# Kernel optimization log

Measured on AMD Instinct MI355X. Metric: run time of the kernel, lower is better.

## Reference

```python
import jax, jax.numpy as jnp
import numpy as np

H, HKV, DH = 16, 8, 128
G = H // HKV
EPS = 1e-6
ROPE_THETA = 1000000.0


def _rms_norm(x, w):
    # RMSNorm over last dim (head_dim)
    var = jnp.mean(x * x, axis=-1, keepdims=True)
    return x * jax.lax.rsqrt(var + EPS) * w


def _rotate_half(x):
    x1, x2 = jnp.split(x, 2, axis=-1)
    return jnp.concatenate([-x2, x1], axis=-1)


def setup_inputs() -> dict:
    key = jax.random.key(0)
    ks = jax.random.split(key, 5)
    B, T, D = 2, 2048, 2048
    s = 0.02
    return {
        "x": jax.random.normal(ks[0], (B, T, D), jnp.float32),
        "wq": jax.random.normal(ks[1], (H * DH, D), jnp.float32) * s,
        "wk": jax.random.normal(ks[2], (HKV * DH, D), jnp.float32) * s,
        "wv": jax.random.normal(ks[3], (HKV * DH, D), jnp.float32) * s,
        "wo": jax.random.normal(ks[4], (D, H * DH), jnp.float32) * s,
        "q_norm_w": jnp.ones((DH,), jnp.float32),
        "k_norm_w": jnp.ones((DH,), jnp.float32),
    }


def reference(x, wq, wk, wv, wo, q_norm_w, k_norm_w):
    B, T, D = x.shape
    # projections (nn.Linear: y = x @ W^T)
    q = (x @ wq.T).reshape(B, T, H, DH).transpose(0, 2, 1, 3)      # [B,H,T,Dh]
    k = (x @ wk.T).reshape(B, T, HKV, DH).transpose(0, 2, 1, 3)    # [B,Hkv,T,Dh]
    v = (x @ wv.T).reshape(B, T, HKV, DH).transpose(0, 2, 1, 3)    # [B,Hkv,T,Dh]

    # QK RMSNorm
    q = _rms_norm(q, q_norm_w)
    k = _rms_norm(k, k_norm_w)

    # RoPE (half-split style), positions 0..T-1
    inv_freq = 1.0 / (ROPE_THETA ** (jnp.arange(0, DH, 2, dtype=jnp.float32) / DH))
    freqs = jnp.arange(T, dtype=jnp.float32)[:, None] * inv_freq[None, :]   # [T,Dh/2]
    emb = jnp.concatenate([freqs, freqs], axis=-1)                           # [T,Dh]
    cos = jnp.cos(emb)[None, None, :, :]
    sin = jnp.sin(emb)[None, None, :, :]
    q = q * cos + _rotate_half(q) * sin
    k = k * cos + _rotate_half(k) * sin

    # GQA attention with fp32 scores and causal mask
    qg = q.reshape(B, HKV, G, T, DH)
    scores = jnp.einsum("bhgtd,bhkd->bhgtk", qg.astype(jnp.float32),
                        k.astype(jnp.float32)) / jnp.sqrt(jnp.float32(DH))
    causal = jnp.tril(jnp.ones((T, T), dtype=bool))[None, None, None, :, :]
    scores = jnp.where(causal, scores, jnp.finfo(jnp.float32).min)
    attn = jax.nn.softmax(scores, axis=-1).astype(x.dtype)
    ctx = jnp.einsum("bhgtk,bhkd->bhgtd", attn, v)                            # [B,Hkv,G,T,Dh]
    out = ctx.reshape(B, H, T, DH).transpose(0, 2, 1, 3).reshape(B, T, H * DH)
    return out @ wo.T
```

## Files before the change

### kernel.cpp

```cpp
#include <hip/hip_runtime.h>
#include <cstdint>

#define Hq 16
#define HKVn 8
#define DHn 128
#define Tn 2048
#define Bn 2
#define Dm 2048
#define BT (Bn*Tn)

typedef __attribute__((ext_vector_type(8))) short bfrag8;
typedef __attribute__((ext_vector_type(4))) float facc4;
typedef __attribute__((ext_vector_type(4))) _Float16 f16x4;
typedef __attribute__((ext_vector_type(8))) _Float16 f16x8;

__device__ __forceinline__ unsigned short f2bf(float f) {
    union { float f; unsigned int u; } v; v.f = f;
    unsigned int u = v.u;
    unsigned int r = (u + 0x7FFFu + ((u >> 16) & 1u)) >> 16;
    return (unsigned short)r;
}

__global__ __launch_bounds__(256) void cvt_kernel(const float* __restrict__ in,
                                                  unsigned short* __restrict__ out, int n4) {
    int i = blockIdx.x * 256 + threadIdx.x;
    if (i < n4) {
        float4 x = ((const float4*)in)[i];
        ushort4 y;
        y.x = f2bf(x.x); y.y = f2bf(x.y); y.z = f2bf(x.z); y.w = f2bf(x.w);
        ((ushort4*)out)[i] = y;
    }
}

__global__ __launch_bounds__(256) void gemm_bt(const unsigned short* __restrict__ A,
                                               const unsigned short* __restrict__ Bm,
                                               float* __restrict__ C,
                                               int M, int N, int K) {
    __shared__ char smem[16384];
    int tid = threadIdx.x;
    int w = tid >> 6, lane = tid & 63, quad = lane >> 4, l15 = lane & 15;
    int wr = w >> 1, wc = w & 1;
    int rowBase = blockIdx.y * 128, colBase = blockIdx.x * 128;
    facc4 acc[4][4];
#pragma unroll
    for (int i = 0; i < 4; i++)
#pragma unroll
        for (int j = 0; j < 4; j++) acc[i][j] = facc4{0.f, 0.f, 0.f, 0.f};

    for (int k0 = 0; k0 < K; k0 += 32) {
        __syncthreads();
#pragma unroll
        for (int issue = 0; issue < 2; issue++) {
            int idx = issue * 256 + tid;
            const unsigned short* ga = A + (size_t)(rowBase + (idx >> 2)) * K + k0 + (idx & 3) * 8;
            __builtin_amdgcn_global_load_lds((const __attribute__((address_space(1))) void*)ga,
                (__attribute__((address_space(3))) void*)(smem + issue * 4096 + w * 1024), 16, 0, 0);
            const unsigned short* gb = Bm + (size_t)(colBase + (idx >> 2)) * K + k0 + (idx & 3) * 8;
            __builtin_amdgcn_global_load_lds((const __attribute__((address_space(1))) void*)gb,
                (__attribute__((address_space(3))) void*)(smem + 8192 + issue * 4096 + w * 1024), 16, 0, 0);
        }
        __syncthreads();
        bfrag8 af[4], bf[4];
#pragma unroll
        for (int i = 0; i < 4; i++)
            af[i] = *(const bfrag8*)(smem + ((wr * 64 + i * 16 + l15) * 32 + quad * 8) * 2);
#pragma unroll
        for (int j = 0; j < 4; j++)
            bf[j] = *(const bfrag8*)(smem + 8192 + ((wc * 64 + j * 16 + l15) * 32 + quad * 8) * 2);
#pragma unroll
        for (int i = 0; i < 4; i++)
#pragma unroll
            for (int j = 0; j < 4; j++)
                acc[i][j] = __builtin_amdgcn_mfma_f32_16x16x32_bf16(af[i], bf[j], acc[i][j], 0, 0, 0);
    }
#pragma unroll
    for (int i = 0; i < 4; i++)
#pragma unroll
        for (int j = 0; j < 4; j++)
#pragma unroll
            for (int r = 0; r < 4; r++) {
                int row = rowBase + wr * 64 + i * 16 + quad * 4 + r;
                int col = colBase + wc * 64 + j * 16 + l15;
                C[(size_t)row * N + col] = acc[i][j][r];
            }
}

__device__ __forceinline__ size_t koff_tiled(int t, int d) {
    int kc = (t >> 4) & 3, l15 = t & 15;
    int f = d >> 5, qd = (d >> 3) & 3, j = d & 7;
    return (size_t)(t >> 6) * 8192 + ((((kc * 4 + f) * 64 + qd * 16 + l15) << 3) + j);
}

__global__ __launch_bounds__(256) void normrope_kernel(const float* __restrict__ qkv,
                                                       const float* __restrict__ qw,
                                                       const float* __restrict__ kw,
                                                       unsigned short* __restrict__ q_bf,
                                                       unsigned short* __restrict__ k_bf) {
    int gw = (blockIdx.x * 256 + threadIdx.x) >> 6;
    int lane = threadIdx.x & 63;
    const float* src; const float* wn; float scale; int t;
    bool isq = (gw < BT * Hq);
    unsigned short* qdst = nullptr; unsigned short* kbase = nullptr;
    if (isq) {
        int bt = gw >> 4, h = gw & 15;
        int b = bt >> 11; t = bt & 2047;
        src = qkv + (size_t)bt * 4096 + h * 128;
        qdst = q_bf + ((size_t)(b * Hq + h) * Tn + t) * 128;
        wn = qw; scale = 0.08838834764831845f;
    } else {
        int g2 = gw - BT * Hq;
        int bt = g2 >> 3, hk = g2 & 7;
        int b = bt >> 11; t = bt & 2047;
        src = qkv + (size_t)bt * 4096 + 2048 + hk * 128;
        kbase = k_bf + (size_t)(b * HKVn + hk) * Tn * 128;
        wn = kw; scale = 1.0f;
    }
    float x0 = src[lane], x1 = src[lane + 64];
    float ss = x0 * x0 + x1 * x1;
#pragma unroll
    for (int off = 32; off > 0; off >>= 1) ss += __shfl_xor(ss, off);
    float inv = rsqrtf(ss * (1.0f / 128.0f) + 1e-6f);
    float n0 = x0 * inv * wn[lane];
    float n1 = x1 * inv * wn[lane + 64];
    float fr = exp2f(-(float)lane * 0.3114307588956902f);
    float ang = (float)t * fr;
    float c = cosf(ang), s = sinf(ang);
    float y0 = (n0 * c - n1 * s) * scale;
    float y1 = (n1 * c + n0 * s) * scale;
    if (isq) {
        qdst[lane] = f2bf(y0);
        qdst[lane + 64] = f2bf(y1);
    } else {
        kbase[koff_tiled(t, lane)] = f2bf(y0);
        kbase[koff_tiled(t, lane + 64)] = f2bf(y1);
    }
}

__global__ __launch_bounds__(256) void vtrans_kernel(const float* __restrict__ qkv,
                                                     _Float16* __restrict__ vT) {
    __shared__ _Float16 tile[64 * 128];
    int tid = threadIdx.x;
    int t64 = blockIdx.x & 31, hk = (blockIdx.x >> 5) & 7, b = blockIdx.x >> 8;
    int t0 = t64 * 64;
#pragma unroll
    for (int i = 0; i < 8; i++) {
        int ix = i * 256 + tid;
        int tl = ix >> 5, dc = (ix & 31) * 4;
        float4 v = *(const float4*)(qkv + (size_t)(b * Tn + t0 + tl) * 4096 + 3072 + hk * 128 + dc);
        tile[tl * 128 + dc + 0] = (_Float16)v.x;
        tile[tl * 128 + dc + 1] = (_Float16)v.y;
        tile[tl * 128 + dc + 2] = (_Float16)v.z;
        tile[tl * 128 + dc + 3] = (_Float16)v.w;
    }
    __syncthreads();
    _Float16* out = vT + (((size_t)(b * HKVn + hk) * 32 + t64) * 8192);
#pragma unroll
    for (int i = 0; i < 4; i++) {
        int oc = i * 256 + tid;
        int dblk = oc >> 7, kcp = (oc >> 6) & 1, qd = (oc >> 4) & 3, l15 = oc & 15;
        f16x8 st;
#pragma unroll
        for (int e = 0; e < 8; e++) {
            int hh = e >> 2, jj = e & 3;
            int t = kcp * 32 + hh * 16 + qd * 4 + jj;
            int d = dblk * 16 + l15;
            st[e] = tile[t * 128 + d];
        }
        *(f16x8*)(out + oc * 8) = st;
    }
}

__global__ __launch_bounds__(256, 2) void attn_kernel(const unsigned short* __restrict__ q_bf,
                                                      const unsigned short* __restrict__ k_glob,
                                                      const _Float16* __restrict__ v_glob,
                                                      unsigned short* __restrict__ ctx) {
    __shared__ char smem[65536];
    int tid = threadIdx.x;
    int w = tid >> 6, lane = tid & 63, quad = lane >> 4, l15 = lane & 15;
    int bid = blockIdx.x;
    int u = bid & 255, halfg = bid >> 8;
    int j = u & 7, h = (u >> 3) & 15, b = (u >> 7) & 1;
    int qblk = halfg ? j : 15 - j;
    int hkv = h >> 1;
    int qb = qblk * 128;
    int qw0 = qb + w * 32;

    const unsigned short* qp = q_bf + (size_t)(b * Hq + h) * Tn * 128;
    const unsigned short* ktile = k_glob + (size_t)(b * HKVn + hkv) * 32 * 8192;
    const _Float16* vtile = v_glob + (size_t)(b * HKVn + hkv) * 32 * 8192;

    bfrag8 qf[2][4];
#pragma unroll
    for (int g = 0; g < 2; g++) {
        int row = qw0 + g * 16 + l15;
#pragma unroll
        for (int f = 0; f < 4; f++)
            qf[g][f] = *(const bfrag8*)(qp + (size_t)row * 128 + f * 32 + quad * 8);
    }

    facc4 o0[8], o1[8];
#pragma unroll
    for (int jj = 0; jj < 8; jj++) { o0[jj] = facc4{0.f,0.f,0.f,0.f}; o1[jj] = facc4{0.f,0.f,0.f,0.f}; }
    float m0 = -__builtin_inff(), m1 = -__builtin_inff(), l0 = 0.f, l1 = 0.f;

    int nkb = qb / 64 + 2;

    {
#pragma unroll
        for (int i = 0; i < 4; i++) {
            const unsigned short* gk = ktile + (size_t)(i * 256 + tid) * 8;
            __builtin_amdgcn_global_load_lds((const __attribute__((address_space(1))) void*)gk,
                (__attribute__((address_space(3))) void*)(smem + i * 4096 + w * 1024), 16, 0, 0);
            const _Float16* gv = vtile + (size_t)(i * 256 + tid) * 8;
            __builtin_amdgcn_global_load_lds((const __attribute__((address_space(1))) void*)gv,
                (__attribute__((address_space(3))) void*)(smem + 16384 + i * 4096 + w * 1024), 16, 0, 0);
        }
    }

    for (int ib = 0; ib < nkb; ib++) {
        int kb = ib * 64;
        __syncthreads();
        if (ib + 1 < nkb) {
            char* nb = smem + ((ib + 1) & 1) * 32768;
#pragma unroll
            for (int i = 0; i < 4; i++) {
                const unsigned short* gk = ktile + (size_t)(ib + 1) * 8192 + (i * 256 + tid) * 8;
                __builtin_amdgcn_global_load_lds((const __attribute__((address_space(1))) void*)gk,
                    (__attribute__((address_space(3))) void*)(nb + i * 4096 + w * 1024), 16, 0, 0);
                const _Float16* gv = vtile + (size_t)(ib + 1) * 8192 + (i * 256 + tid) * 8;
                __builtin_amdgcn_global_load_lds((const __attribute__((address_space(1))) void*)gv,
                    (__attribute__((address_space(3))) void*)(nb + 16384 + i * 4096 + w * 1024), 16, 0, 0);
            }
        }
        char* cb = smem + (ib & 1) * 32768;
        if (kb <= qw0 + 31) {
            facc4 s0[4], s1[4];
#pragma unroll
            for (int kc = 0; kc < 4; kc++) {
                bfrag8 kf[4];
#pragma unroll
                for (int f = 0; f < 4; f++)
                    kf[f] = *(const bfrag8*)(cb + (((kc * 4 + f) * 64 + lane) << 4));
                facc4 a = facc4{0.f,0.f,0.f,0.f}, bq = facc4{0.f,0.f,0.f,0.f};
#pragma unroll
                for (int f = 0; f < 4; f++) {
                    a  = __builtin_amdgcn_mfma_f32_16x16x32_bf16(kf[f], qf[0][f], a, 0, 0, 0);
                    bq = __builtin_amdgcn_mfma_f32_16x16x32_bf16(kf[f], qf[1][f], bq, 0, 0, 0);
                }
                s0[kc] = a; s1[kc] = bq;
            }
            if (kb + 63 > qw0) {
                int q0 = qw0 + l15, q1 = q0 + 16;
#pragma unroll
                for (int kc = 0; kc < 4; kc++)
#pragma unroll
                    for (int r = 0; r < 4; r++) {
                        int k = kb + kc * 16 + quad * 4 + r;
                        if (k > q0) s0[kc][r] = -__builtin_inff();
                        if (k > q1) s1[kc][r] = -__builtin_inff();
                    }
            }
            float mx0 = s0[0][0], mx1 = s1[0][0];
#pragma unroll
            for (int kc = 0; kc < 4; kc++)
#pragma unroll
                for (int r = 0; r < 4; r++) {
                    mx0 = fmaxf(mx0, s0[kc][r]); mx1 = fmaxf(mx1, s1[kc][r]);
                }
            mx0 = fmaxf(mx0, __shfl_xor(mx0, 16)); mx0 = fmaxf(mx0, __shfl_xor(mx0, 32));
            mx1 = fmaxf(mx1, __shfl_xor(mx1, 16)); mx1 = fmaxf(mx1, __shfl_xor(mx1, 32));
            float mn0 = fmaxf(m0, mx0), mn1 = fmaxf(m1, mx1);
            float alpha0 = __expf(m0 - mn0), alpha1 = __expf(m1 - mn1);
            m0 = mn0; m1 = mn1;
            float rs0 = 0.f, rs1 = 0.f;
#pragma unroll
            for (int kc = 0; kc < 4; kc++)
#pragma unroll
                for (int r = 0; r < 4; r++) {
                    s0[kc][r] = __expf(s0[kc][r] - m0); rs0 += s0[kc][r];
                    s1[kc][r] = __expf(s1[kc][r] - m1); rs1 += s1[kc][r];
                }
            rs0 += __shfl_xor(rs0, 16); rs0 += __shfl_xor(rs0, 32);
            rs1 += __shfl_xor(rs1, 16); rs1 += __shfl_xor(rs1, 32);
            l0 = l0 * alpha0 + rs0; l1 = l1 * alpha1 + rs1;
#pragma unroll
            for (int jj = 0; jj < 8; jj++)
#pragma unroll
                for (int r = 0; r < 4; r++) { o0[jj][r] *= alpha0; o1[jj][r] *= alpha1; }
            f16x4 pb0[4], pb1[4];
#pragma unroll
            for (int kc = 0; kc < 4; kc++) {
                pb0[kc] = f16x4{(_Float16)s0[kc][0], (_Float16)s0[kc][1],
                                (_Float16)s0[kc][2], (_Float16)s0[kc][3]};
                pb1[kc] = f16x4{(_Float16)s1[kc][0], (_Float16)s1[kc][1],
                                (_Float16)s1[kc][2], (_Float16)s1[kc][3]};
            }
#pragma unroll
            for (int kcp = 0; kcp < 2; kcp++)
#pragma unroll
                for (int dblk = 0; dblk < 8; dblk++) {
                    f16x8 vv = *(const f16x8*)(cb + 16384 + (((dblk * 2 + kcp) * 64 + lane) << 4));
                    f16x4 a0 = f16x4{vv[0], vv[1], vv[2], vv[3]};
                    f16x4 a1 = f16x4{vv[4], vv[5], vv[6], vv[7]};
                    o0[dblk] = __builtin_amdgcn_mfma_f32_16x16x16f16(a0, pb0[kcp*2],   o0[dblk], 0, 0, 0);
                    o0[dblk] = __builtin_amdgcn_mfma_f32_16x16x16f16(a1, pb0[kcp*2+1], o0[dblk], 0, 0, 0);
                    o1[dblk] = __builtin_amdgcn_mfma_f32_16x16x16f16(a0, pb1[kcp*2],   o1[dblk], 0, 0, 0);
                    o1[dblk] = __builtin_amdgcn_mfma_f32_16x16x16f16(a1, pb1[kcp*2+1], o1[dblk], 0, 0, 0);
                }
        }
    }
    float inv0 = 1.0f / l0, inv1 = 1.0f / l1;
#pragma unroll
    for (int g = 0; g < 2; g++) {
        int q = qw0 + g * 16 + l15;
        float invl = g ? inv1 : inv0;
#pragma unroll
        for (int dblk = 0; dblk < 8; dblk++) {
            facc4 ov = g ? o1[dblk] : o0[dblk];
            ushort4 st;
            st.x = f2bf(ov[0] * invl); st.y = f2bf(ov[1] * invl);
            st.z = f2bf(ov[2] * invl); st.w = f2bf(ov[3] * invl);
            *(ushort4*)(ctx + ((size_t)(b * Tn + q)) * 2048 + h * 128 + dblk * 16 + quad * 4) = st;
        }
    }
}

extern "C" void kernel_launch(void* const* d_in, const int* in_sizes, int n_in,
                              void* d_out, int out_size, void* d_ws, size_t ws_size,
                              hipStream_t stream) {
    (void)in_sizes; (void)n_in; (void)out_size; (void)ws_size;
    const float* x  = (const float*)d_in[0];
    const float* wq = (const float*)d_in[1];
    const float* wk = (const float*)d_in[2];
    const float* wv = (const float*)d_in[3];
    const float* wo = (const float*)d_in[4];
    const float* qw = (const float*)d_in[5];
    const float* kw = (const float*)d_in[6];
    float* out = (float*)d_out;
    char* ws = (char*)d_ws;

    unsigned short* x_bf    = (unsigned short*)(ws);
    unsigned short* wqkv_bf = (unsigned short*)(ws + 16777216);
    unsigned short* wo_bf   = (unsigned short*)(ws + 33554432);
    float*          qkv_f   = (float*)(ws + 41943040);
    unsigned short* q_bf    = (unsigned short*)(ws + 109051904);
    unsigned short* k_bf    = (unsigned short*)(ws + 125829120);
    _Float16*       vT_f16  = (_Float16*)(ws + 134217728);
    unsigned short* ctx_bf  = (unsigned short*)(ws + 142606336);

    cvt_kernel<<<8192, 256, 0, stream>>>(x, x_bf, 2097152);
    cvt_kernel<<<4096, 256, 0, stream>>>(wq, wqkv_bf, 1048576);
    cvt_kernel<<<2048, 256, 0, stream>>>(wk, wqkv_bf + 4194304, 524288);
    cvt_kernel<<<2048, 256, 0, stream>>>(wv, wqkv_bf + 6291456, 524288);
    cvt_kernel<<<4096, 256, 0, stream>>>(wo, wo_bf, 1048576);
    gemm_bt<<<dim3(32, 32), 256, 0, stream>>>(x_bf, wqkv_bf, qkv_f, 4096, 4096, 2048);
    normrope_kernel<<<24576, 256, 0, stream>>>(qkv_f, qw, kw, q_bf, k_bf);
    vtrans_kernel<<<512, 256, 0, stream>>>(qkv_f, vT_f16);
    attn_kernel<<<512, 256, 0, stream>>>(q_bf, k_bf, vT_f16, ctx_bf);
    gemm_bt<<<dim3(16, 32), 256, 0, stream>>>(ctx_bf, wo_bf, out, 4096, 2048, 2048);
}
```

Measured before the change: 374.9 us.

## Fuse QK norm, RoPE and V transpose into QKV GEMM epilogue; merge conversions

```diff
diff --git a/kernel.cpp b/kernel.cpp
--- a/kernel.cpp
+++ b/kernel.cpp
@@ -13,6 +13,7 @@
 typedef __attribute__((ext_vector_type(4))) float facc4;
 typedef __attribute__((ext_vector_type(4))) _Float16 f16x4;
 typedef __attribute__((ext_vector_type(8))) _Float16 f16x8;
+typedef __attribute__((ext_vector_type(8))) unsigned short us8;
 
 __device__ __forceinline__ unsigned short f2bf(float f) {
     union { float f; unsigned int u; } v; v.f = f;
@@ -20,23 +21,43 @@
     unsigned int r = (u + 0x7FFFu + ((u >> 16) & 1u)) >> 16;
     return (unsigned short)r;
 }
-
-__global__ __launch_bounds__(256) void cvt_kernel(const float* __restrict__ in,
-                                                  unsigned short* __restrict__ out, int n4) {
+__device__ __forceinline__ float bf2f(unsigned short u) {
+    union { unsigned int u; float f; } v; v.u = ((unsigned int)u) << 16;
+    return v.f;
+}
+
+__global__ __launch_bounds__(256) void cvt_all(const float* __restrict__ x,
+                                               const float* __restrict__ wq,
+                                               const float* __restrict__ wk,
+                                               const float* __restrict__ wv,
+                                               const float* __restrict__ wo,
+                                               unsigned short* __restrict__ x_bf,
+                                               unsigned short* __restrict__ wqkv_bf,
+                                               unsigned short* __restrict__ wo_bf) {
     int i = blockIdx.x * 256 + threadIdx.x;
-    if (i < n4) {
-        float4 x = ((const float4*)in)[i];
-        ushort4 y;
-        y.x = f2bf(x.x); y.y = f2bf(x.y); y.z = f2bf(x.z); y.w = f2bf(x.w);
-        ((ushort4*)out)[i] = y;
-    }
+    const float4* src; ushort4* dst;
+    if (i < 2097152)      { src = (const float4*)x  + i;            dst = (ushort4*)x_bf + i; }
+    else if (i < 3145728) { src = (const float4*)wq + (i-2097152);  dst = (ushort4*)wqkv_bf + (i-2097152); }
+    else if (i < 3670016) { src = (const float4*)wk + (i-3145728);  dst = (ushort4*)wqkv_bf + 1048576 + (i-3145728); }
+    else if (i < 4194304) { src = (const float4*)wv + (i-3670016);  dst = (ushort4*)wqkv_bf + 1572864 + (i-3670016); }
+    else                  { src = (const float4*)wo + (i-4194304);  dst = (ushort4*)wo_bf + (i-4194304); }
+    float4 v = *src;
+    ushort4 y;
+    y.x = f2bf(v.x); y.y = f2bf(v.y); y.z = f2bf(v.z); y.w = f2bf(v.w);
+    *dst = y;
+}
+
+__device__ __forceinline__ size_t koff_tiled(int t, int d) {
+    int kc = (t >> 4) & 3, l15 = t & 15;
+    int f = d >> 5, qd = (d >> 3) & 3, j = d & 7;
+    return (size_t)(t >> 6) * 8192 + ((((kc * 4 + f) * 64 + qd * 16 + l15) << 3) + j);
 }
 
 __global__ __launch_bounds__(256) void gemm_bt(const unsigned short* __restrict__ A,
                                                const unsigned short* __restrict__ Bm,
                                                float* __restrict__ C,
                                                int M, int N, int K) {
-    __shared__ char smem[16384];
+    __shared__ char smem[32768];
     int tid = threadIdx.x;
     int w = tid >> 6, lane = tid & 63, quad = lane >> 4, l15 = lane & 15;
     int wr = w >> 1, wc = w & 1;
@@ -47,31 +68,41 @@
 #pragma unroll
         for (int j = 0; j < 4; j++) acc[i][j] = facc4{0.f, 0.f, 0.f, 0.f};
 
-    for (int k0 = 0; k0 < K; k0 += 32) {
+    for (int k0 = 0; k0 < K; k0 += 64) {
         __syncthreads();
 #pragma unroll
-        for (int issue = 0; issue < 2; issue++) {
-            int idx = issue * 256 + tid;
-            const unsigned short* ga = A + (size_t)(rowBase + (idx >> 2)) * K + k0 + (idx & 3) * 8;
+        for (int i4 = 0; i4 < 4; i4++) {
+            int c = i4 * 256 + tid;
+            int r = c >> 3, kkg = (c & 7) ^ (r & 7);
+            const unsigned short* ga = A + (size_t)(rowBase + r) * K + k0 + kkg * 8;
             __builtin_amdgcn_global_load_lds((const __attribute__((address_space(1))) void*)ga,
-                (__attribute__((address_space(3))) void*)(smem + issue * 4096 + w * 1024), 16, 0, 0);
-            const unsigned short* gb = Bm + (size_t)(colBase + (idx >> 2)) * K + k0 + (idx & 3) * 8;
+                (__attribute__((address_space(3))) void*)(smem + i4 * 4096 + w * 1024), 16, 0, 0);
+            const unsigned short* gb = Bm + (size_t)(colBase + r) * K + k0 + kkg * 8;
             __builtin_amdgcn_global_load_lds((const __attribute__((address_space(1))) void*)gb,
-                (__attribute__((address_space(3))) void*)(smem + 8192 + issue * 4096 + w * 1024), 16, 0, 0);
+                (__attribute__((address_space(3))) void*)(smem + 16384 + i4 * 4096 + w * 1024), 16, 0, 0);
         }
         __syncthreads();
-        bfrag8 af[4], bf[4];
-#pragma unroll
-        for (int i = 0; i < 4; i++)
-            af[i] = *(const bfrag8*)(smem + ((wr * 64 + i * 16 + l15) * 32 + quad * 8) * 2);
-#pragma unroll
-        for (int j = 0; j < 4; j++)
-            bf[j] = *(const bfrag8*)(smem + 8192 + ((wc * 64 + j * 16 + l15) * 32 + quad * 8) * 2);
-#pragma unroll
-        for (int i = 0; i < 4; i++)
-#pragma unroll
-            for (int j = 0; j < 4; j++)
-                acc[i][j] = __builtin_amdgcn_mfma_f32_16x16x32_bf16(af[i], bf[j], acc[i][j], 0, 0, 0);
+#pragma unroll
+        for (int kh = 0; kh < 2; kh++) {
+            bfrag8 af[4], bf[4];
+#pragma unroll
+            for (int i = 0; i < 4; i++) {
+                int row = wr * 64 + i * 16 + l15;
+                int ch = row * 8 + ((kh * 4 + quad) ^ (row & 7));
+                af[i] = *(const bfrag8*)(smem + ch * 16);
+            }
+#pragma unroll
+            for (int j = 0; j < 4; j++) {
+                int row = wc * 64 + j * 16 + l15;
+                int ch = row * 8 + ((kh * 4 + quad) ^ (row & 7));
+                bf[j] = *(const bfrag8*)(smem + 16384 + ch * 16);
+            }
+#pragma unroll
+            for (int i = 0; i < 4; i++)
+#pragma unroll
+                for (int j = 0; j < 4; j++)
+                    acc[i][j] = __builtin_amdgcn_mfma_f32_16x16x32_bf16(af[i], bf[j], acc[i][j], 0, 0, 0);
+        }
     }
 #pragma unroll
     for (int i = 0; i < 4; i++)
@@ -85,88 +116,154 @@
             }
 }
 
-__device__ __forceinline__ size_t koff_tiled(int t, int d) {
-    int kc = (t >> 4) & 3, l15 = t & 15;
-    int f = d >> 5, qd = (d >> 3) & 3, j = d & 7;
-    return (size_t)(t >> 6) * 8192 + ((((kc * 4 + f) * 64 + qd * 16 + l15) << 3) + j);
-}
-
-__global__ __launch_bounds__(256) void normrope_kernel(const float* __restrict__ qkv,
-                                                       const float* __restrict__ qw,
-                                                       const float* __restrict__ kw,
-                                                       unsigned short* __restrict__ q_bf,
-                                                       unsigned short* __restrict__ k_bf) {
-    int gw = (blockIdx.x * 256 + threadIdx.x) >> 6;
-    int lane = threadIdx.x & 63;
-    const float* src; const float* wn; float scale; int t;
-    bool isq = (gw < BT * Hq);
-    unsigned short* qdst = nullptr; unsigned short* kbase = nullptr;
-    if (isq) {
-        int bt = gw >> 4, h = gw & 15;
-        int b = bt >> 11; t = bt & 2047;
-        src = qkv + (size_t)bt * 4096 + h * 128;
-        qdst = q_bf + ((size_t)(b * Hq + h) * Tn + t) * 128;
-        wn = qw; scale = 0.08838834764831845f;
-    } else {
-        int g2 = gw - BT * Hq;
-        int bt = g2 >> 3, hk = g2 & 7;
-        int b = bt >> 11; t = bt & 2047;
-        src = qkv + (size_t)bt * 4096 + 2048 + hk * 128;
-        kbase = k_bf + (size_t)(b * HKVn + hk) * Tn * 128;
-        wn = kw; scale = 1.0f;
-    }
-    float x0 = src[lane], x1 = src[lane + 64];
-    float ss = x0 * x0 + x1 * x1;
-#pragma unroll
-    for (int off = 32; off > 0; off >>= 1) ss += __shfl_xor(ss, off);
-    float inv = rsqrtf(ss * (1.0f / 128.0f) + 1e-6f);
-    float n0 = x0 * inv * wn[lane];
-    float n1 = x1 * inv * wn[lane + 64];
-    float fr = exp2f(-(float)lane * 0.3114307588956902f);
-    float ang = (float)t * fr;
-    float c = cosf(ang), s = sinf(ang);
-    float y0 = (n0 * c - n1 * s) * scale;
-    float y1 = (n1 * c + n0 * s) * scale;
-    if (isq) {
-        qdst[lane] = f2bf(y0);
-        qdst[lane + 64] = f2bf(y1);
-    } else {
-        kbase[koff_tiled(t, lane)] = f2bf(y0);
-        kbase[koff_tiled(t, lane + 64)] = f2bf(y1);
-    }
-}
-
-__global__ __launch_bounds__(256) void vtrans_kernel(const float* __restrict__ qkv,
-                                                     _Float16* __restrict__ vT) {
-    __shared__ _Float16 tile[64 * 128];
+__global__ __launch_bounds__(256) void gemm_qkv_fused(const unsigned short* __restrict__ A,
+                                                      const unsigned short* __restrict__ Bm,
+                                                      const float* __restrict__ qw,
+                                                      const float* __restrict__ kw,
+                                                      unsigned short* __restrict__ q_bf,
+                                                      unsigned short* __restrict__ k_bf,
+                                                      _Float16* __restrict__ vT) {
+    __shared__ char smem[35840];
+    const int K = 2048, Nn = 4096;
     int tid = threadIdx.x;
-    int t64 = blockIdx.x & 31, hk = (blockIdx.x >> 5) & 7, b = blockIdx.x >> 8;
-    int t0 = t64 * 64;
-#pragma unroll
-    for (int i = 0; i < 8; i++) {
-        int ix = i * 256 + tid;
-        int tl = ix >> 5, dc = (ix & 31) * 4;
-        float4 v = *(const float4*)(qkv + (size_t)(b * Tn + t0 + tl) * 4096 + 3072 + hk * 128 + dc);
-        tile[tl * 128 + dc + 0] = (_Float16)v.x;
-        tile[tl * 128 + dc + 1] = (_Float16)v.y;
-        tile[tl * 128 + dc + 2] = (_Float16)v.z;
-        tile[tl * 128 + dc + 3] = (_Float16)v.w;
+    int w = tid >> 6, lane = tid & 63, quad = lane >> 4, l15 = lane & 15;
+    int wr = w >> 1, wc = w & 1;
+    int bx = blockIdx.x;
+    int rowBase = blockIdx.y * 128, colBase = bx * 128;
+    (void)Nn;
+    facc4 acc[4][4];
+#pragma unroll
+    for (int i = 0; i < 4; i++)
+#pragma unroll
+        for (int j = 0; j < 4; j++) acc[i][j] = facc4{0.f, 0.f, 0.f, 0.f};
+
+    for (int k0 = 0; k0 < K; k0 += 64) {
+        __syncthreads();
+#pragma unroll
+        for (int i4 = 0; i4 < 4; i4++) {
+            int c = i4 * 256 + tid;
+            int r = c >> 3, kkg = (c & 7) ^ (r & 7);
+            const unsigned short* ga = A + (size_t)(rowBase + r) * K + k0 + kkg * 8;
+            __builtin_amdgcn_global_load_lds((const __attribute__((address_space(1))) void*)ga,
+                (__attribute__((address_space(3))) void*)(smem + i4 * 4096 + w * 1024), 16, 0, 0);
+            const unsigned short* gb = Bm + (size_t)(colBase + r) * K + k0 + kkg * 8;
+            __builtin_amdgcn_global_load_lds((const __attribute__((address_space(1))) void*)gb,
+                (__attribute__((address_space(3))) void*)(smem + 16384 + i4 * 4096 + w * 1024), 16, 0, 0);
+        }
+        __syncthreads();
+#pragma unroll
+        for (int kh = 0; kh < 2; kh++) {
+            bfrag8 af[4], bf[4];
+#pragma unroll
+            for (int i = 0; i < 4; i++) {
+                int row = wr * 64 + i * 16 + l15;
+                int ch = row * 8 + ((kh * 4 + quad) ^ (row & 7));
+                af[i] = *(const bfrag8*)(smem + ch * 16);
+            }
+#pragma unroll
+            for (int j = 0; j < 4; j++) {
+                int row = wc * 64 + j * 16 + l15;
+                int ch = row * 8 + ((kh * 4 + quad) ^ (row & 7));
+                bf[j] = *(const bfrag8*)(smem + 16384 + ch * 16);
+            }
+#pragma unroll
+            for (int i = 0; i < 4; i++)
+#pragma unroll
+                for (int j = 0; j < 4; j++)
+                    acc[i][j] = __builtin_amdgcn_mfma_f32_16x16x32_bf16(af[i], bf[j], acc[i][j], 0, 0, 0);
+        }
+    }
+
+    if (bx >= 24) {
+        int hv = bx - 24;
+        int gt0 = rowBase + wr * 64;
+        int bb = gt0 >> 11;
+        int t64 = (gt0 & 2047) >> 6;
+        _Float16* base = vT + ((size_t)(bb * 8 + hv) * 32 + t64) * 8192;
+#pragma unroll
+        for (int i = 0; i < 4; i++) {
+            int kcp = i >> 1, hh = i & 1;
+#pragma unroll
+            for (int j = 0; j < 4; j++) {
+                int dblk = wc * 4 + j;
+                f16x4 pv;
+#pragma unroll
+                for (int r = 0; r < 4; r++) pv[r] = (_Float16)acc[i][j][r];
+                *(f16x4*)(base + (((dblk * 2 + kcp) * 64 + quad * 16 + l15) * 8) + hh * 4) = pv;
+            }
+        }
+        return;
+    }
+
+    const float* wn = (bx < 16) ? qw : kw;
+    const float osc = (bx < 16) ? (0.08838834764831845f * 1.4426950408889634f) : 1.0f;
+    float* sums = (float*)(smem + 34816);
+    float ssum[4][4];
+#pragma unroll
+    for (int i = 0; i < 4; i++)
+#pragma unroll
+        for (int r = 0; r < 4; r++) {
+            float s = 0.f;
+#pragma unroll
+            for (int j = 0; j < 4; j++) s += acc[i][j][r] * acc[i][j][r];
+            s += __shfl_xor(s, 1); s += __shfl_xor(s, 2);
+            s += __shfl_xor(s, 4); s += __shfl_xor(s, 8);
+            ssum[i][r] = s;
+        }
+    if (l15 == 0) {
+#pragma unroll
+        for (int i = 0; i < 4; i++)
+#pragma unroll
+            for (int r = 0; r < 4; r++)
+                sums[wc * 128 + wr * 64 + i * 16 + quad * 4 + r] = ssum[i][r];
     }
     __syncthreads();
-    _Float16* out = vT + (((size_t)(b * HKVn + hk) * 32 + t64) * 8192);
-#pragma unroll
-    for (int i = 0; i < 4; i++) {
-        int oc = i * 256 + tid;
-        int dblk = oc >> 7, kcp = (oc >> 6) & 1, qd = (oc >> 4) & 3, l15 = oc & 15;
-        f16x8 st;
-#pragma unroll
-        for (int e = 0; e < 8; e++) {
-            int hh = e >> 2, jj = e & 3;
-            int t = kcp * 32 + hh * 16 + qd * 4 + jj;
-            int d = dblk * 16 + l15;
-            st[e] = tile[t * 128 + d];
-        }
-        *(f16x8*)(out + oc * 8) = st;
+    unsigned short* tile = (unsigned short*)smem;
+    float wcol[4];
+#pragma unroll
+    for (int j = 0; j < 4; j++) wcol[j] = wn[wc * 64 + j * 16 + l15];
+#pragma unroll
+    for (int i = 0; i < 4; i++)
+#pragma unroll
+        for (int r = 0; r < 4; r++) {
+            int row = wr * 64 + i * 16 + quad * 4 + r;
+            float tot = sums[row] + sums[128 + row];
+            float inv = rsqrtf(tot * (1.0f / 128.0f) + 1e-6f);
+#pragma unroll
+            for (int j = 0; j < 4; j++)
+                tile[row * 136 + wc * 64 + j * 16 + l15] = f2bf(acc[i][j][r] * inv * wcol[j]);
+        }
+    __syncthreads();
+    {
+        int row = tid >> 1, d0 = (tid & 1) * 32;
+        int gt = rowBase + row;
+        int t = gt & 2047, bb = gt >> 11;
+        unsigned short* qrow = q_bf + ((size_t)(bb * 16 + bx) * 2048 + t) * 128;
+        unsigned short* kplane = k_bf + (size_t)(bb * 8 + (bx - 16)) * 2048 * 128;
+        float tf = (float)t;
+#pragma unroll
+        for (int dc = 0; dc < 32; dc += 8) {
+            int db = d0 + dc;
+            us8 n0u = *(const us8*)(tile + row * 136 + db);
+            us8 n1u = *(const us8*)(tile + row * 136 + db + 64);
+            us8 p0, p1;
+#pragma unroll
+            for (int e = 0; e < 8; e++) {
+                float fr = exp2f(-(float)(db + e) * 0.3114307588956902f);
+                float sv, cv;
+                __sincosf(tf * fr, &sv, &cv);
+                float a0 = bf2f(n0u[e]), a1 = bf2f(n1u[e]);
+                p0[e] = f2bf((a0 * cv - a1 * sv) * osc);
+                p1[e] = f2bf((a1 * cv + a0 * sv) * osc);
+            }
+            if (bx < 16) {
+                *(us8*)(qrow + db) = p0;
+                *(us8*)(qrow + db + 64) = p1;
+            } else {
+                *(us8*)(kplane + koff_tiled(t, db)) = p0;
+                *(us8*)(kplane + koff_tiled(t, db + 64)) = p1;
+            }
+        }
     }
 }
 
@@ -204,17 +301,14 @@
     float m0 = -__builtin_inff(), m1 = -__builtin_inff(), l0 = 0.f, l1 = 0.f;
 
     int nkb = qb / 64 + 2;
-
-    {
-#pragma unroll
-        for (int i = 0; i < 4; i++) {
-            const unsigned short* gk = ktile + (size_t)(i * 256 + tid) * 8;
-            __builtin_amdgcn_global_load_lds((const __attribute__((address_space(1))) void*)gk,
-                (__attribute__((address_space(3))) void*)(smem + i * 4096 + w * 1024), 16, 0, 0);
-            const _Float16* gv = vtile + (size_t)(i * 256 + tid) * 8;
-            __builtin_amdgcn_global_load_lds((const __attribute__((address_space(1))) void*)gv,
-                (__attribute__((address_space(3))) void*)(smem + 16384 + i * 4096 + w * 1024), 16, 0, 0);
-        }
+#pragma unroll
+    for (int i = 0; i < 4; i++) {
+        const unsigned short* gk = ktile + (size_t)(i * 256 + tid) * 8;
+        __builtin_amdgcn_global_load_lds((const __attribute__((address_space(1))) void*)gk,
+            (__attribute__((address_space(3))) void*)(smem + i * 4096 + w * 1024), 16, 0, 0);
+        const _Float16* gv = vtile + (size_t)(i * 256 + tid) * 8;
+        __builtin_amdgcn_global_load_lds((const __attribute__((address_space(1))) void*)gv,
+            (__attribute__((address_space(3))) void*)(smem + 16384 + i * 4096 + w * 1024), 16, 0, 0);
     }
 
     for (int ib = 0; ib < nkb; ib++) {
@@ -270,15 +364,15 @@
             mx0 = fmaxf(mx0, __shfl_xor(mx0, 16)); mx0 = fmaxf(mx0, __shfl_xor(mx0, 32));
             mx1 = fmaxf(mx1, __shfl_xor(mx1, 16)); mx1 = fmaxf(mx1, __shfl_xor(mx1, 32));
             float mn0 = fmaxf(m0, mx0), mn1 = fmaxf(m1, mx1);
-            float alpha0 = __expf(m0 - mn0), alpha1 = __expf(m1 - mn1);
+            float alpha0 = exp2f(m0 - mn0), alpha1 = exp2f(m1 - mn1);
             m0 = mn0; m1 = mn1;
             float rs0 = 0.f, rs1 = 0.f;
 #pragma unroll
             for (int kc = 0; kc < 4; kc++)
 #pragma unroll
                 for (int r = 0; r < 4; r++) {
-                    s0[kc][r] = __expf(s0[kc][r] - m0); rs0 += s0[kc][r];
-                    s1[kc][r] = __expf(s1[kc][r] - m1); rs1 += s1[kc][r];
+                    s0[kc][r] = exp2f(s0[kc][r] - m0); rs0 += s0[kc][r];
+                    s1[kc][r] = exp2f(s1[kc][r] - m1); rs1 += s1[kc][r];
                 }
             rs0 += __shfl_xor(rs0, 16); rs0 += __shfl_xor(rs0, 32);
             rs1 += __shfl_xor(rs1, 16); rs1 += __shfl_xor(rs1, 32);
@@ -342,20 +436,13 @@
     unsigned short* x_bf    = (unsigned short*)(ws);
     unsigned short* wqkv_bf = (unsigned short*)(ws + 16777216);
     unsigned short* wo_bf   = (unsigned short*)(ws + 33554432);
-    float*          qkv_f   = (float*)(ws + 41943040);
-    unsigned short* q_bf    = (unsigned short*)(ws + 109051904);
-    unsigned short* k_bf    = (unsigned short*)(ws + 125829120);
-    _Float16*       vT_f16  = (_Float16*)(ws + 134217728);
-    unsigned short* ctx_bf  = (unsigned short*)(ws + 142606336);
-
-    cvt_kernel<<<8192, 256, 0, stream>>>(x, x_bf, 2097152);
-    cvt_kernel<<<4096, 256, 0, stream>>>(wq, wqkv_bf, 1048576);
-    cvt_kernel<<<2048, 256, 0, stream>>>(wk, wqkv_bf + 4194304, 524288);
-    cvt_kernel<<<2048, 256, 0, stream>>>(wv, wqkv_bf + 6291456, 524288);
-    cvt_kernel<<<4096, 256, 0, stream>>>(wo, wo_bf, 1048576);
-    gemm_bt<<<dim3(32, 32), 256, 0, stream>>>(x_bf, wqkv_bf, qkv_f, 4096, 4096, 2048);
-    normrope_kernel<<<24576, 256, 0, stream>>>(qkv_f, qw, kw, q_bf, k_bf);
-    vtrans_kernel<<<512, 256, 0, stream>>>(qkv_f, vT_f16);
+    unsigned short* q_bf    = (unsigned short*)(ws + 41943040);
+    unsigned short* k_bf    = (unsigned short*)(ws + 58720256);
+    _Float16*       vT_f16  = (_Float16*)(ws + 67108864);
+    unsigned short* ctx_bf  = (unsigned short*)(ws + 75497472);
+
+    cvt_all<<<20480, 256, 0, stream>>>(x, wq, wk, wv, wo, x_bf, wqkv_bf, wo_bf);
+    gemm_qkv_fused<<<dim3(32, 32), 256, 0, stream>>>(x_bf, wqkv_bf, qw, kw, q_bf, k_bf, vT_f16);
     attn_kernel<<<512, 256, 0, stream>>>(q_bf, k_bf, vT_f16, ctx_bf);
     gemm_bt<<<dim3(16, 32), 256, 0, stream>>>(ctx_bf, wo_bf, out, 4096, 2048, 2048);
 }
```

Measured after the change: 331.7 us. -11.5%, faster.
